# Optimization experiments

Hardware: AMD Instinct MI355X
Metric: run time of the kernel (lower is better)

The kernel has to match this reference:

```python
import jax, jax.numpy as jnp
import numpy as np

HEADS = 16

def rotate_half(t):
    t1, t2 = jnp.split(t, 2, axis=-1)
    return jnp.concatenate([-t2, t1], axis=-1)

def apply_rotary_pos_emb(pos, t):
    # pos: [N, hd] broadcasts against t: [B, H, N, hd]
    return t * jnp.cos(pos) + rotate_half(t) * jnp.sin(pos)

def setup_inputs() -> dict:
    key = jax.random.key(0)
    ks = jax.random.split(key, 6)
    B, N, D, H = 2, 2048, 1024, HEADS
    hd = D // H
    s = D ** -0.5
    x = jax.random.normal(ks[0], (B, N, D), jnp.float32)
    context = jax.random.normal(ks[1], (B, N, D), jnp.float32)
    pos_emb = jax.random.normal(ks[2], (N, hd), jnp.float32)
    Wq = jax.random.normal(ks[3], (D, D), jnp.float32) * s
    Wkv = jax.random.normal(ks[4], (D, 2 * D), jnp.float32) * s
    Wout = jax.random.normal(ks[5], (D, D), jnp.float32) * s
    b_out = jnp.zeros((D,), jnp.float32)
    return {"x": x, "context": context, "pos_emb": pos_emb,
            "Wq": Wq, "Wkv": Wkv, "Wout": Wout, "b_out": b_out}

def reference(x, context, pos_emb, Wq, Wkv, Wout, b_out):
    B, N, D = x.shape
    H = HEADS
    hd = D // H
    scale = hd ** -0.5
    # projections: [B,N,D] -> [B,H,N,hd]
    q = (x @ Wq).reshape(B, N, H, hd).transpose(0, 2, 1, 3)
    k, v = jnp.split(context @ Wkv, 2, axis=-1)
    k = k.reshape(B, N, H, hd).transpose(0, 2, 1, 3)
    v = v.reshape(B, N, H, hd).transpose(0, 2, 1, 3)
    # rotary applied to q and k just before scores
    q = apply_rotary_pos_emb(pos_emb, q)
    k = apply_rotary_pos_emb(pos_emb, k)
    dots = jnp.einsum('bhid,bhjd->bhij', q, k) * scale  # [B,H,N,N]
    attn = jax.nn.softmax(dots, axis=-1)
    out = jnp.einsum('bhij,bhjd->bhid', attn, v)
    out = out.transpose(0, 2, 1, 3).reshape(B, N, D)
    return out @ Wout + b_out
```

## Files before the change

### kernel.cpp

```cpp
#include <hip/hip_runtime.h>
#include <math.h>

#define D_MODEL 1024
#define NSEQ    2048
#define NHEADS  16
#define HD      64

typedef __attribute__((ext_vector_type(8))) short bf16x8;
typedef __attribute__((ext_vector_type(4))) float f32x4;

__device__ inline unsigned short f2bf(float x) {
    union { float f; unsigned int u; } a; a.f = x;
    unsigned int r = a.u + 0x7fffu + ((a.u >> 16) & 1u);
    return (unsigned short)(r >> 16);
}
__device__ inline float bf2f(unsigned short b) {
    union { unsigned int u; float f; } a; a.u = ((unsigned int)b) << 16;
    return a.f;
}
__device__ inline unsigned int pack2(unsigned short a, unsigned short b) {
    return (unsigned int)a | ((unsigned int)b << 16);
}
__device__ inline unsigned int cvtpk_bf16(float lo, float hi) {
    unsigned int r;
    asm volatile("v_cvt_pk_bf16_f32 %0, %1, %2" : "=v"(r) : "v"(lo), "v"(hi));
    return r;
}
__device__ inline float fexp2(float x) { return __builtin_amdgcn_exp2f(x); }
__device__ inline void async_load16(const void* g, void* l) {
    __builtin_amdgcn_global_load_lds(
        (const __attribute__((address_space(1))) unsigned int*)g,
        (__attribute__((address_space(3))) unsigned int*)l, 16, 0, 0);
}

#define QSCALE 0.180336880111112f
#define MSHIFT 12.0f

__global__ __launch_bounds__(256) void prep_kernel(
    const float* __restrict__ x, const float* __restrict__ ctx,
    const float* __restrict__ Wq, const float* __restrict__ Wkv,
    const float* __restrict__ Wout, const float* __restrict__ pos,
    unsigned short* __restrict__ AX, unsigned short* __restrict__ AC,
    unsigned short* __restrict__ WQ, unsigned short* __restrict__ WK,
    unsigned short* __restrict__ WO, float* __restrict__ ct,
    float* __restrict__ st)
{
    __shared__ float Ws[32][33];
    const int bid = blockIdx.x, tid = threadIdx.x;
    if (bid < 8192) {
        const float* src = bid < 4096 ? x : ctx;
        unsigned short* dst = bid < 4096 ? AX : AC;
        int m = bid & 4095;
        int kq = tid * 4;
        float4 v = *reinterpret_cast<const float4*>(&src[(size_t)m * 1024 + kq]);
        float vv[4] = {v.x, v.y, v.z, v.w};
        unsigned short h[4];
#pragma unroll
        for (int c = 0; c < 4; ++c) h[c] = f2bf(vv[c]);
        size_t base = (size_t)m * 2048 + kq;
        *reinterpret_cast<uint2*>(&dst[base]) =
            make_uint2(pack2(h[0], h[1]), pack2(h[2], h[3]));
    } else if (bid < 12288) {
        int t = bid - 8192;
        const float* W; unsigned short* Y; int N, tilesx;
        if (t < 1024)      { W = Wq;   Y = WQ; N = 1024; tilesx = 32; }
        else if (t < 3072) { t -= 1024; W = Wkv; Y = WK; N = 2048; tilesx = 64; }
        else               { t -= 3072; W = Wout; Y = WO; N = 1024; tilesx = 32; }
        int n0 = (t % tilesx) * 32, k0 = (t / tilesx) * 32;
        int c = tid & 31, r4 = tid >> 5;
#pragma unroll
        for (int i = 0; i < 4; ++i) {
            int r = r4 * 4 + i;
            Ws[r][c] = W[(size_t)(k0 + r) * N + n0 + c];
        }
        __syncthreads();
#pragma unroll
        for (int i = 0; i < 4; ++i) {
            int nr = r4 * 4 + i;
            Y[(size_t)(n0 + nr) * 2048 + k0 + c] = f2bf(Ws[c][nr]);
        }
    } else {
        int idx = (bid - 12288) * 256 + tid;
        float s, c;
        sincosf(pos[idx], &s, &c);
        ct[idx] = c;
        st[idx] = s;
    }
}

__global__ __launch_bounds__(512) void gemm_qkv(
    const unsigned short* __restrict__ AX, const unsigned short* __restrict__ AC,
    const unsigned short* __restrict__ WQ, const unsigned short* __restrict__ WK,
    unsigned short* __restrict__ Qb, unsigned short* __restrict__ Kb,
    unsigned short* __restrict__ Vt, const float* __restrict__ ct,
    const float* __restrict__ st)
{
    __shared__ unsigned short As[128 * 64];
    __shared__ unsigned short Bs[128 * 64];
    const int tid = threadIdx.x;
    const int l = tid & 63;
    const int wv = tid >> 6;
    const int wr  = wv >> 2;
    const int wch = (wv & 3) >> 1;
    const int whf = wv & 1;
    const int lr_ = l & 15, lg_ = l >> 4;

    const unsigned short *A, *Bt;
    int row0, col0, isQ;
    if (blockIdx.x < 256) {
        A = AX; Bt = WQ; isQ = 1;
        col0 = (blockIdx.x & 7) * 128;
        row0 = (blockIdx.x >> 3) * 128;
    } else {
        int i2 = blockIdx.x - 256;
        A = AC; Bt = WK; isQ = 0;
        int x = i2 & 7, i = i2 >> 3;
        col0 = (x * 2 + (i & 1)) * 128;
        row0 = (i >> 1) * 128;
    }

    f32x4 acc[4][2];
#pragma unroll
    for (int m = 0; m < 4; ++m)
#pragma unroll
        for (int n = 0; n < 2; ++n) acc[m][n] = (f32x4){0.f, 0.f, 0.f, 0.f};

    const int rsub = l >> 3;
    const int chst = (l & 7) ^ rsub;

    for (int k0 = 0; k0 < 1024; k0 += 64) {
        __syncthreads();
#pragma unroll
        for (int t = 0; t < 2; ++t) {
            int ci = wv * 2 + t;
            int row = ci * 8 + rsub;
            async_load16(&A[(size_t)(row0 + row) * 2048 + k0 + chst * 8],
                         &As[ci * 512]);
            async_load16(&Bt[(size_t)(col0 + row) * 2048 + k0 + chst * 8],
                         &Bs[ci * 512]);
        }
        __syncthreads();
#pragma unroll
        for (int ks = 0; ks < 2; ++ks) {
            int ch2 = (lg_ + ks * 4) ^ (lr_ & 7);
            bf16x8 af[4], bfv[2];
#pragma unroll
            for (int m = 0; m < 4; ++m)
                af[m] = *reinterpret_cast<const bf16x8*>(
                    &As[(wr * 64 + m * 16 + lr_) * 64 + ch2 * 8]);
#pragma unroll
            for (int n = 0; n < 2; ++n)
                bfv[n] = *reinterpret_cast<const bf16x8*>(
                    &Bs[(wch * 64 + whf * 16 + n * 32 + lr_) * 64 + ch2 * 8]);
#pragma unroll
            for (int m = 0; m < 4; ++m)
#pragma unroll
                for (int n = 0; n < 2; ++n)
                    acc[m][n] = __builtin_amdgcn_mfma_f32_16x16x32_bf16(
                        af[m], bfv[n], acc[m][n], 0, 0, 0);
        }
    }

    const int colw = col0 + wch * 64;
    if (isQ || colw < 1024) {
        unsigned short* dst = isQ ? Qb : Kb;
        const int hh = colw >> 6;
        const float qs = isQ ? QSCALE : 1.f;
#pragma unroll
        for (int m = 0; m < 4; ++m) {
            int grow0 = row0 + wr * 64 + m * 16 + lg_ * 4;
            int b = grow0 >> 11, nq0 = grow0 & 2047;
#pragma unroll
            for (int j = 0; j < 4; ++j) {
                int nq = nq0 + j;
                int d = whf * 16 + lr_;
                float a = acc[m][0][j], bb = acc[m][1][j];
                float c1 = ct[nq * 64 + d],      s1 = st[nq * 64 + d];
                float c2 = ct[nq * 64 + d + 32], s2 = st[nq * 64 + d + 32];
                size_t obase = (((size_t)b * 16 + hh) * 2048 + nq) * 64;
                dst[obase + d]      = f2bf((a * c1 - bb * s1) * qs);
                dst[obase + d + 32] = f2bf((bb * c2 + a * s2) * qs);
            }
        }
    } else {
        const int hh = (colw - 1024) >> 6;
#pragma unroll
        for (int m = 0; m < 4; ++m) {
            int grow0 = row0 + wr * 64 + m * 16 + lg_ * 4;
            int b = grow0 >> 11, nq0 = grow0 & 2047;
#pragma unroll
            for (int n = 0; n < 2; ++n) {
                int d = whf * 16 + n * 32 + lr_;
                unsigned int w0 = pack2(f2bf(acc[m][n][0]), f2bf(acc[m][n][1]));
                unsigned int w1 = pack2(f2bf(acc[m][n][2]), f2bf(acc[m][n][3]));
                *reinterpret_cast<uint2*>(
                    &Vt[(((size_t)b * 16 + hh) * 64 + d) * 2048 + nq0]) =
                    make_uint2(w0, w1);
            }
        }
    }
}

__global__ __launch_bounds__(512) void gemm_out(
    const unsigned short* __restrict__ A, const unsigned short* __restrict__ Bt,
    const float* __restrict__ bias, float* __restrict__ C)
{
    __shared__ unsigned short As[128 * 64];
    __shared__ unsigned short Bs[128 * 64];
    const int tid = threadIdx.x;
    const int l = tid & 63;
    const int wv = tid >> 6;
    const int wr  = wv >> 2;
    const int wch = (wv & 3) >> 1;
    const int whf = wv & 1;
    const int lr_ = l & 15, lg_ = l >> 4;
    const int col0 = (blockIdx.x & 7) * 128;
    const int row0 = (blockIdx.x >> 3) * 128;

    f32x4 acc[4][2];
#pragma unroll
    for (int m = 0; m < 4; ++m)
#pragma unroll
        for (int n = 0; n < 2; ++n) acc[m][n] = (f32x4){0.f, 0.f, 0.f, 0.f};

    const int rsub = l >> 3;
    const int chst = (l & 7) ^ rsub;

    for (int k0 = 0; k0 < 1024; k0 += 64) {
        __syncthreads();
#pragma unroll
        for (int t = 0; t < 2; ++t) {
            int ci = wv * 2 + t;
            int row = ci * 8 + rsub;
            async_load16(&A[(size_t)(row0 + row) * 2048 + k0 + chst * 8],
                         &As[ci * 512]);
            async_load16(&Bt[(size_t)(col0 + row) * 2048 + k0 + chst * 8],
                         &Bs[ci * 512]);
        }
        __syncthreads();
#pragma unroll
        for (int ks = 0; ks < 2; ++ks) {
            int ch2 = (lg_ + ks * 4) ^ (lr_ & 7);
            bf16x8 af[4], bfv[2];
#pragma unroll
            for (int m = 0; m < 4; ++m)
                af[m] = *reinterpret_cast<const bf16x8*>(
                    &As[(wr * 64 + m * 16 + lr_) * 64 + ch2 * 8]);
#pragma unroll
            for (int n = 0; n < 2; ++n)
                bfv[n] = *reinterpret_cast<const bf16x8*>(
                    &Bs[(wch * 64 + whf * 16 + n * 32 + lr_) * 64 + ch2 * 8]);
#pragma unroll
            for (int m = 0; m < 4; ++m)
#pragma unroll
                for (int n = 0; n < 2; ++n)
                    acc[m][n] = __builtin_amdgcn_mfma_f32_16x16x32_bf16(
                        af[m], bfv[n], acc[m][n], 0, 0, 0);
        }
    }

#pragma unroll
    for (int m = 0; m < 4; ++m) {
        int grow0 = row0 + wr * 64 + m * 16 + lg_ * 4;
#pragma unroll
        for (int n = 0; n < 2; ++n) {
            int gcol = col0 + wch * 64 + whf * 16 + n * 32 + lr_;
            float bv = bias[gcol];
#pragma unroll
            for (int j = 0; j < 4; ++j)
                C[(size_t)(grow0 + j) * 1024 + gcol] = acc[m][n][j] + bv;
        }
    }
}

__global__ __launch_bounds__(512) void flash_mfma(
    const unsigned short* __restrict__ Qb, const unsigned short* __restrict__ Kb,
    const unsigned short* __restrict__ Vt, unsigned short* __restrict__ Oa)
{
    __shared__ unsigned short Ks[2][4096];
    __shared__ unsigned short Vs[2][4096];
    __shared__ unsigned short Ps[8][1024];

    const int tid = threadIdx.x;
    const int l = tid & 63;
    const int w = tid >> 6;
    const int lg = l >> 4;
    const int lr = l & 15;
    const int bh = blockIdx.y;
    const int q0 = blockIdx.x * 128;

    bf16x8 qf[2];
    {
        const unsigned short* qp =
            Qb + ((size_t)bh * NSEQ + q0 + w * 16 + lr) * HD + lg * 8;
        qf[0] = *reinterpret_cast<const bf16x8*>(qp);
        qf[1] = *reinterpret_cast<const bf16x8*>(qp + 32);
    }

    f32x4 oacc[4];
#pragma unroll
    for (int j = 0; j < 4; ++j) oacc[j] = (f32x4){0.f, 0.f, 0.f, 0.f};
    float l_i = 0.f;

    unsigned short* pw = Ps[w];

    const int r_  = tid >> 3;
    const int ch_ = (tid & 7) ^ (r_ & 7);
    const unsigned short* kPtr = Kb + ((size_t)bh * NSEQ + r_) * HD + ch_ * 8;
    const unsigned short* vPtr = Vt + ((size_t)bh * HD + r_) * NSEQ + ch_ * 8;

#define STAGE(b) do {                              \
    async_load16(kPtr, &Ks[b][w * 512]);           \
    async_load16(vPtr, &Vs[b][w * 512]);           \
    kPtr += 64 * HD; vPtr += 64;                   \
} while (0)

#define COMPUTE(b) do {                                                        \
    f32x4 sacc[4];                                                             \
    _Pragma("unroll")                                                          \
    for (int n = 0; n < 4; ++n)                                                \
        sacc[n] = (f32x4){-MSHIFT, -MSHIFT, -MSHIFT, -MSHIFT};                 \
    __builtin_amdgcn_s_setprio(1);                                             \
    _Pragma("unroll")                                                          \
    for (int ks = 0; ks < 2; ++ks)                                             \
        _Pragma("unroll")                                                      \
        for (int n = 0; n < 4; ++n) {                                          \
            int kr = n * 16 + lr;                                              \
            int ch = (lg + ks * 4) ^ (kr & 7);                                 \
            bf16x8 kf = *reinterpret_cast<const bf16x8*>(                      \
                &Ks[b][kr * 64 + ch * 8]);                                     \
            sacc[n] = __builtin_amdgcn_mfma_f32_16x16x32_bf16(                 \
                kf, qf[ks], sacc[n], 0, 0, 0);                                 \
        }                                                                      \
    __builtin_amdgcn_s_setprio(0);                                             \
    float p[4][4];                                                             \
    float sum = 0.f;                                                           \
    _Pragma("unroll")                                                          \
    for (int n = 0; n < 4; ++n)                                                \
        _Pragma("unroll")                                                      \
        for (int j = 0; j < 4; ++j) {                                          \
            p[n][j] = fexp2(sacc[n][j]);                                       \
            sum += p[n][j];                                                    \
        }                                                                      \
    sum += __shfl_xor(sum, 16);                                                \
    sum += __shfl_xor(sum, 32);                                                \
    l_i += sum;                                                                \
    _Pragma("unroll")                                                          \
    for (int n = 0; n < 4; ++n) {                                              \
        unsigned int u0 = cvtpk_bf16(p[n][0], p[n][1]);                        \
        unsigned int u1 = cvtpk_bf16(p[n][2], p[n][3]);                        \
        int swc = (2 * n + (lg >> 1)) ^ (lr & 7);                              \
        *reinterpret_cast<uint2*>(&pw[lr * 64 + swc * 8 + 4 * (lg & 1)]) =     \
            make_uint2(u0, u1);                                                \
    }                                                                          \
    asm volatile("s_waitcnt lgkmcnt(0)" ::: "memory");                         \
    __builtin_amdgcn_s_setprio(1);                                             \
    _Pragma("unroll")                                                          \
    for (int ks = 0; ks < 2; ++ks) {                                           \
        int pch = (lg + 4 * ks) ^ (lr & 7);                                    \
        bf16x8 pf = *reinterpret_cast<const bf16x8*>(                          \
            &pw[lr * 64 + pch * 8]);                                           \
        _Pragma("unroll")                                                      \
        for (int dt = 0; dt < 4; ++dt) {                                       \
            int d = dt * 16 + lr;                                              \
            int ch = (lg + ks * 4) ^ (d & 7);                                  \
            bf16x8 vf = *reinterpret_cast<const bf16x8*>(                      \
                &Vs[b][d * 64 + ch * 8]);                                      \
            oacc[dt] = __builtin_amdgcn_mfma_f32_16x16x32_bf16(                \
                pf, vf, oacc[dt], 0, 0, 0);                                    \
        }                                                                      \
    }                                                                          \
    __builtin_amdgcn_s_setprio(0);                                             \
} while (0)

    STAGE(0);
    asm volatile("s_waitcnt vmcnt(0)" ::: "memory");
    __syncthreads();

    for (int jt = 0; jt < NSEQ / 64; jt += 2) {
        STAGE(1);
        COMPUTE(0);
        asm volatile("s_waitcnt vmcnt(0)" ::: "memory");
        __syncthreads();
        if (jt + 2 < NSEQ / 64) STAGE(0);
        COMPUTE(1);
        asm volatile("s_waitcnt vmcnt(0)" ::: "memory");
        __syncthreads();
    }
#undef STAGE
#undef COMPUTE

    const int b = bh >> 4, h = bh & 15;
#pragma unroll
    for (int j = 0; j < 4; ++j) {
        float lj = __shfl(l_i, (l & 48) | (lg * 4 + j));
        float inv = 1.f / lj;
        int nq = q0 + w * 16 + lg * 4 + j;
        size_t rbase = ((size_t)b * NSEQ + nq) * 2048 + h * 64;
#pragma unroll
        for (int dt = 0; dt < 4; ++dt)
            Oa[rbase + dt * 16 + lr] = f2bf(oacc[dt][j] * inv);
    }
}

__global__ __launch_bounds__(256) void sgemm_kernel(
    const float* __restrict__ A, const float* __restrict__ B,
    const float* __restrict__ bias, float* __restrict__ C,
    int M, int N, int K)
{
    __shared__ float As[16][132];
    __shared__ float Bs[16][132];
    const int tid = threadIdx.x;
    const int tr = tid >> 4;
    const int tc = tid & 15;
    const int arow0 = blockIdx.y * 128;
    const int bcol0 = blockIdx.x * 128;
    float acc[8][8];
#pragma unroll
    for (int i = 0; i < 8; ++i)
#pragma unroll
        for (int j = 0; j < 8; ++j) acc[i][j] = 0.f;
    for (int k0 = 0; k0 < K; k0 += 16) {
#pragma unroll
        for (int t = 0; t < 2; ++t) {
            int f = tid + t * 256;
            int row = f >> 2, kg = f & 3;
            float4 av = *reinterpret_cast<const float4*>(
                &A[(size_t)(arow0 + row) * K + k0 + kg * 4]);
            As[kg * 4 + 0][row] = av.x;
            As[kg * 4 + 1][row] = av.y;
            As[kg * 4 + 2][row] = av.z;
            As[kg * 4 + 3][row] = av.w;
        }
#pragma unroll
        for (int t = 0; t < 2; ++t) {
            int f = tid + t * 256;
            int kr = f >> 5, cg = f & 31;
            *reinterpret_cast<float4*>(&Bs[kr][cg * 4]) =
                *reinterpret_cast<const float4*>(
                    &B[(size_t)(k0 + kr) * N + bcol0 + cg * 4]);
        }
        __syncthreads();
#pragma unroll
        for (int kk = 0; kk < 16; ++kk) {
            float a[8], b[8];
            *reinterpret_cast<float4*>(&a[0]) = *reinterpret_cast<const float4*>(&As[kk][tr * 4]);
            *reinterpret_cast<float4*>(&a[4]) = *reinterpret_cast<const float4*>(&As[kk][64 + tr * 4]);
            *reinterpret_cast<float4*>(&b[0]) = *reinterpret_cast<const float4*>(&Bs[kk][tc * 4]);
            *reinterpret_cast<float4*>(&b[4]) = *reinterpret_cast<const float4*>(&Bs[kk][64 + tc * 4]);
#pragma unroll
            for (int i = 0; i < 8; ++i)
#pragma unroll
                for (int j = 0; j < 8; ++j) acc[i][j] = fmaf(a[i], b[j], acc[i][j]);
        }
        __syncthreads();
    }
#pragma unroll
    for (int i = 0; i < 8; ++i) {
        int row = arow0 + ((i < 4) ? (tr * 4 + i) : (64 + tr * 4 + i - 4));
#pragma unroll
        for (int jh = 0; jh < 2; ++jh) {
            int col = bcol0 + ((jh == 0) ? (tc * 4) : (64 + tc * 4));
            float4 v;
            v.x = acc[i][jh * 4 + 0];
            v.y = acc[i][jh * 4 + 1];
            v.z = acc[i][jh * 4 + 2];
            v.w = acc[i][jh * 4 + 3];
            if (bias) {
                v.x += bias[col + 0]; v.y += bias[col + 1];
                v.z += bias[col + 2]; v.w += bias[col + 3];
            }
            *reinterpret_cast<float4*>(&C[(size_t)row * N + col]) = v;
        }
    }
}

__global__ void rope_kernel(float* __restrict__ t, const float* __restrict__ pos,
                            int rowstride)
{
    int idx = blockIdx.x * 256 + threadIdx.x;
    int d = idx & 31;
    int h = (idx >> 5) & (NHEADS - 1);
    int m = idx >> 9;
    int n = m & (NSEQ - 1);
    float p1 = pos[n * HD + d];
    float p2 = pos[n * HD + 32 + d];
    size_t base = (size_t)m * rowstride + h * HD;
    float a = t[base + d];
    float b = t[base + 32 + d];
    float s1, c1, s2, c2;
    sincosf(p1, &s1, &c1);
    sincosf(p2, &s2, &c2);
    t[base + d]      = a * c1 - b * s1;
    t[base + 32 + d] = b * c2 + a * s2;
}

__global__ __launch_bounds__(256) void flash_kernel(
    const float* __restrict__ q, const float* __restrict__ kv,
    float* __restrict__ o)
{
    __shared__ float Qs[64][68];
    __shared__ float Kt[64][68];
    __shared__ float Vs2[64][68];

    const int rb = blockIdx.x;
    const int bh = blockIdx.y;
    const int b = bh >> 4;
    const int h = bh & (NHEADS - 1);
    const int tid = threadIdx.x;
    const int tr = tid >> 4;
    const int tc = tid & 15;

#pragma unroll
    for (int t = 0; t < 4; ++t) {
        int f = tid + t * 256;
        int row = f >> 4, cg = f & 15;
        *reinterpret_cast<float4*>(&Qs[row][cg * 4]) =
            *reinterpret_cast<const float4*>(
                &q[((size_t)(b * NSEQ + rb * 64 + row)) * D_MODEL + h * HD + cg * 4]);
    }

    float m_i[4], l_i[4], oacc[4][4];
#pragma unroll
    for (int i = 0; i < 4; ++i) {
        m_i[i] = -INFINITY; l_i[i] = 0.f;
#pragma unroll
        for (int j = 0; j < 4; ++j) oacc[i][j] = 0.f;
    }

    float (*Ps2)[68] = Kt;

    for (int jt = 0; jt < NSEQ / 64; ++jt) {
        __syncthreads();
#pragma unroll
        for (int t = 0; t < 4; ++t) {
            int f = tid + t * 256;
            int row = f >> 4, cg = f & 15;
            size_t base = ((size_t)(b * NSEQ + jt * 64 + row)) * (2 * D_MODEL) + h * HD + cg * 4;
            float4 kq = *reinterpret_cast<const float4*>(&kv[base]);
            float4 vv = *reinterpret_cast<const float4*>(&kv[base + D_MODEL]);
            Kt[cg * 4 + 0][row] = kq.x;
            Kt[cg * 4 + 1][row] = kq.y;
            Kt[cg * 4 + 2][row] = kq.z;
            Kt[cg * 4 + 3][row] = kq.w;
            *reinterpret_cast<float4*>(&Vs2[row][cg * 4]) = vv;
        }
        __syncthreads();

        float s[4][4];
#pragma unroll
        for (int i = 0; i < 4; ++i)
#pragma unroll
            for (int j = 0; j < 4; ++j) s[i][j] = 0.f;
        for (int dg = 0; dg < 16; ++dg) {
            float Qv[4][4];
#pragma unroll
            for (int i = 0; i < 4; ++i)
                *reinterpret_cast<float4*>(Qv[i]) =
                    *reinterpret_cast<const float4*>(&Qs[tr * 4 + i][dg * 4]);
#pragma unroll
            for (int dd = 0; dd < 4; ++dd) {
                float ka[4];
                *reinterpret_cast<float4*>(ka) =
                    *reinterpret_cast<const float4*>(&Kt[dg * 4 + dd][tc * 4]);
#pragma unroll
                for (int i = 0; i < 4; ++i)
#pragma unroll
                    for (int j = 0; j < 4; ++j)
                        s[i][j] = fmaf(Qv[i][dd], ka[j], s[i][j]);
            }
        }

#pragma unroll
        for (int i = 0; i < 4; ++i) {
            float tmax = -INFINITY;
#pragma unroll
            for (int j = 0; j < 4; ++j) {
                s[i][j] *= 0.125f;
                tmax = fmaxf(tmax, s[i][j]);
            }
#pragma unroll
            for (int msk = 1; msk < 16; msk <<= 1)
                tmax = fmaxf(tmax, __shfl_xor(tmax, msk, 16));
            float mnew = fmaxf(m_i[i], tmax);
            float corr = expf(m_i[i] - mnew);
            float tsum = 0.f;
#pragma unroll
            for (int j = 0; j < 4; ++j) {
                s[i][j] = expf(s[i][j] - mnew);
                tsum += s[i][j];
            }
#pragma unroll
            for (int msk = 1; msk < 16; msk <<= 1)
                tsum += __shfl_xor(tsum, msk, 16);
            l_i[i] = l_i[i] * corr + tsum;
            m_i[i] = mnew;
#pragma unroll
            for (int j = 0; j < 4; ++j) oacc[i][j] *= corr;
        }

        __syncthreads();
#pragma unroll
        for (int i = 0; i < 4; ++i) {
            float4 v;
            v.x = s[i][0]; v.y = s[i][1]; v.z = s[i][2]; v.w = s[i][3];
            *reinterpret_cast<float4*>(&Ps2[tr * 4 + i][tc * 4]) = v;
        }
        __syncthreads();

        for (int cg = 0; cg < 16; ++cg) {
            float P_[4][4], V_[4][4];
#pragma unroll
            for (int i = 0; i < 4; ++i)
                *reinterpret_cast<float4*>(P_[i]) =
                    *reinterpret_cast<const float4*>(&Ps2[tr * 4 + i][cg * 4]);
#pragma unroll
            for (int c = 0; c < 4; ++c)
                *reinterpret_cast<float4*>(V_[c]) =
                    *reinterpret_cast<const float4*>(&Vs2[cg * 4 + c][tc * 4]);
#pragma unroll
            for (int i = 0; i < 4; ++i)
#pragma unroll
                for (int c = 0; c < 4; ++c)
#pragma unroll
                    for (int j = 0; j < 4; ++j)
                        oacc[i][j] = fmaf(P_[i][c], V_[c][j], oacc[i][j]);
        }
    }

#pragma unroll
    for (int i = 0; i < 4; ++i) {
        float inv = 1.f / l_i[i];
        float4 v;
        v.x = oacc[i][0] * inv; v.y = oacc[i][1] * inv;
        v.z = oacc[i][2] * inv; v.w = oacc[i][3] * inv;
        *reinterpret_cast<float4*>(
            &o[((size_t)(b * NSEQ + rb * 64 + tr * 4 + i)) * D_MODEL + h * HD + tc * 4]) = v;
    }
}

extern "C" void kernel_launch(void* const* d_in, const int* in_sizes, int n_in,
                              void* d_out, int out_size, void* d_ws, size_t ws_size,
                              hipStream_t stream) {
    const float* x       = (const float*)d_in[0];
    const float* context = (const float*)d_in[1];
    const float* pos     = (const float*)d_in[2];
    const float* Wq      = (const float*)d_in[3];
    const float* Wkv     = (const float*)d_in[4];
    const float* Wout    = (const float*)d_in[5];
    const float* b_out   = (const float*)d_in[6];
    float* out = (float*)d_out;

    const int M = 2 * NSEQ;
    dim3 blk(256);

    const size_t NEED = 76546048ULL;
    if (ws_size >= NEED) {
        unsigned short* AX = (unsigned short*)d_ws;
        unsigned short* AC = AX + 8388608;
        unsigned short* WQ = AC + 8388608;
        unsigned short* WK = WQ + 2097152;
        unsigned short* WO = WK + 4194304;
        unsigned short* Qb = WO + 2097152;
        unsigned short* Kb = Qb + 4194304;
        unsigned short* Vt = Kb + 4194304;
        float* ct = (float*)(Vt + 4194304);
        float* st = ct + 131072;

        prep_kernel<<<12800, blk, 0, stream>>>(
            x, context, Wq, Wkv, Wout, pos, AX, AC, WQ, WK, WO, ct, st);
        gemm_qkv<<<768, dim3(512), 0, stream>>>(AX, AC, WQ, WK, Qb, Kb, Vt, ct, st);
        flash_mfma<<<dim3(NSEQ / 128, 32), dim3(512), 0, stream>>>(Qb, Kb, Vt, AX);
        gemm_out<<<256, dim3(512), 0, stream>>>(AX, WO, b_out, out);
    } else {
        float* ws = (float*)d_ws;
        float* q  = ws;
        float* kv = q + (size_t)M * D_MODEL;
        float* o  = kv + (size_t)M * 2 * D_MODEL;
        sgemm_kernel<<<dim3(D_MODEL / 128, M / 128), blk, 0, stream>>>(
            x, Wq, nullptr, q, M, D_MODEL, D_MODEL);
        sgemm_kernel<<<dim3(2 * D_MODEL / 128, M / 128), blk, 0, stream>>>(
            context, Wkv, nullptr, kv, M, 2 * D_MODEL, D_MODEL);
        rope_kernel<<<(M * NHEADS * 32) / 256, blk, 0, stream>>>(q, pos, D_MODEL);
        rope_kernel<<<(M * NHEADS * 32) / 256, blk, 0, stream>>>(kv, pos, 2 * D_MODEL);
        flash_kernel<<<dim3(NSEQ / 64, 2 * NHEADS), blk, 0, stream>>>(q, kv, o);
        sgemm_kernel<<<dim3(D_MODEL / 128, M / 128), blk, 0, stream>>>(
            o, Wout, b_out, out, M, D_MODEL, D_MODEL);
    }
}
```

Measured before the change: 122.8 us.

## Triple-buffer flash K/V loads with single barrier; shrink out-proj GEMM tiles

The attention kernel now uses three shared K/V buffers and a partial vmcnt wait with one barrier per tile, so global loads for the next tile stay in flight while the current tile computes. This removes the full drain and double barrier per iteration. The output projection GEMM switches from 128x128 tiles with 512 threads to 64x64 tiles with 256 threads and four times as many blocks, to fill more CUs. The trade-off is more shared memory per flash block and less data reuse in the GEMM.

After: 118.0 us. 1.04x faster.

```diff
diff --git a/kernel.cpp b/kernel.cpp
--- a/kernel.cpp
+++ b/kernel.cpp
@@ -201,25 +201,24 @@
     }
 }
 
-__global__ __launch_bounds__(512) void gemm_out(
+__global__ __launch_bounds__(256) void gemm_out(
     const unsigned short* __restrict__ A, const unsigned short* __restrict__ Bt,
     const float* __restrict__ bias, float* __restrict__ C)
 {
-    __shared__ unsigned short As[128 * 64];
-    __shared__ unsigned short Bs[128 * 64];
+    __shared__ unsigned short As[64 * 64];
+    __shared__ unsigned short Bs[64 * 64];
     const int tid = threadIdx.x;
     const int l = tid & 63;
     const int wv = tid >> 6;
-    const int wr  = wv >> 2;
-    const int wch = (wv & 3) >> 1;
-    const int whf = wv & 1;
+    const int wr = wv >> 1;
+    const int wp = wv & 1;
     const int lr_ = l & 15, lg_ = l >> 4;
-    const int col0 = (blockIdx.x & 7) * 128;
-    const int row0 = (blockIdx.x >> 3) * 128;
-
-    f32x4 acc[4][2];
-#pragma unroll
-    for (int m = 0; m < 4; ++m)
+    const int row0 = (blockIdx.x >> 4) * 64;
+    const int col0 = (blockIdx.x & 15) * 64;
+
+    f32x4 acc[2][2];
+#pragma unroll
+    for (int m = 0; m < 2; ++m)
 #pragma unroll
         for (int n = 0; n < 2; ++n) acc[m][n] = (f32x4){0.f, 0.f, 0.f, 0.f};
 
@@ -230,7 +229,7 @@
         __syncthreads();
 #pragma unroll
         for (int t = 0; t < 2; ++t) {
-            int ci = wv * 2 + t;
+            int ci = wv + 4 * t;
             int row = ci * 8 + rsub;
             async_load16(&A[(size_t)(row0 + row) * 2048 + k0 + chst * 8],
                          &As[ci * 512]);
@@ -241,17 +240,17 @@
 #pragma unroll
         for (int ks = 0; ks < 2; ++ks) {
             int ch2 = (lg_ + ks * 4) ^ (lr_ & 7);
-            bf16x8 af[4], bfv[2];
-#pragma unroll
-            for (int m = 0; m < 4; ++m)
+            bf16x8 af[2], bfv[2];
+#pragma unroll
+            for (int m = 0; m < 2; ++m)
                 af[m] = *reinterpret_cast<const bf16x8*>(
-                    &As[(wr * 64 + m * 16 + lr_) * 64 + ch2 * 8]);
+                    &As[(wr * 32 + m * 16 + lr_) * 64 + ch2 * 8]);
 #pragma unroll
             for (int n = 0; n < 2; ++n)
                 bfv[n] = *reinterpret_cast<const bf16x8*>(
-                    &Bs[(wch * 64 + whf * 16 + n * 32 + lr_) * 64 + ch2 * 8]);
-#pragma unroll
-            for (int m = 0; m < 4; ++m)
+                    &Bs[(wp * 16 + n * 32 + lr_) * 64 + ch2 * 8]);
+#pragma unroll
+            for (int m = 0; m < 2; ++m)
 #pragma unroll
                 for (int n = 0; n < 2; ++n)
                     acc[m][n] = __builtin_amdgcn_mfma_f32_16x16x32_bf16(
@@ -260,11 +259,11 @@
     }
 
 #pragma unroll
-    for (int m = 0; m < 4; ++m) {
-        int grow0 = row0 + wr * 64 + m * 16 + lg_ * 4;
+    for (int m = 0; m < 2; ++m) {
+        int grow0 = row0 + wr * 32 + m * 16 + lg_ * 4;
 #pragma unroll
         for (int n = 0; n < 2; ++n) {
-            int gcol = col0 + wch * 64 + whf * 16 + n * 32 + lr_;
+            int gcol = col0 + wp * 16 + n * 32 + lr_;
             float bv = bias[gcol];
 #pragma unroll
             for (int j = 0; j < 4; ++j)
@@ -277,8 +276,8 @@
     const unsigned short* __restrict__ Qb, const unsigned short* __restrict__ Kb,
     const unsigned short* __restrict__ Vt, unsigned short* __restrict__ Oa)
 {
-    __shared__ unsigned short Ks[2][4096];
-    __shared__ unsigned short Vs[2][4096];
+    __shared__ unsigned short Ks[3][4096];
+    __shared__ unsigned short Vs[3][4096];
     __shared__ unsigned short Ps[8][1024];
 
     const int tid = threadIdx.x;
@@ -313,6 +312,12 @@
     async_load16(kPtr, &Ks[b][w * 512]);           \
     async_load16(vPtr, &Vs[b][w * 512]);           \
     kPtr += 64 * HD; vPtr += 64;                   \
+} while (0)
+
+#define WAITBAR2 do {                                              \
+    asm volatile("s_waitcnt vmcnt(2)" ::: "memory");               \
+    __builtin_amdgcn_s_barrier();                                  \
+    __builtin_amdgcn_sched_barrier(0);                             \
 } while (0)
 
 #define COMPUTE(b) do {                                                        \
@@ -354,6 +359,7 @@
             make_uint2(u0, u1);                                                \
     }                                                                          \
     asm volatile("s_waitcnt lgkmcnt(0)" ::: "memory");                         \
+    __builtin_amdgcn_sched_barrier(0);                                         \
     __builtin_amdgcn_s_setprio(1);                                             \
     _Pragma("unroll")                                                          \
     for (int ks = 0; ks < 2; ++ks) {                                           \
@@ -374,20 +380,18 @@
 } while (0)
 
     STAGE(0);
+    for (int base = 0; base < 30; base += 3) {
+        STAGE(1); WAITBAR2; COMPUTE(0);
+        STAGE(2); WAITBAR2; COMPUTE(1);
+        STAGE(0); WAITBAR2; COMPUTE(2);
+    }
+    STAGE(1); WAITBAR2; COMPUTE(0);
     asm volatile("s_waitcnt vmcnt(0)" ::: "memory");
-    __syncthreads();
-
-    for (int jt = 0; jt < NSEQ / 64; jt += 2) {
-        STAGE(1);
-        COMPUTE(0);
-        asm volatile("s_waitcnt vmcnt(0)" ::: "memory");
-        __syncthreads();
-        if (jt + 2 < NSEQ / 64) STAGE(0);
-        COMPUTE(1);
-        asm volatile("s_waitcnt vmcnt(0)" ::: "memory");
-        __syncthreads();
-    }
+    __builtin_amdgcn_s_barrier();
+    __builtin_amdgcn_sched_barrier(0);
+    COMPUTE(1);
 #undef STAGE
+#undef WAITBAR2
 #undef COMPUTE
 
     const int b = bh >> 4, h = bh & 15;
@@ -671,7 +675,7 @@
             x, context, Wq, Wkv, Wout, pos, AX, AC, WQ, WK, WO, ct, st);
         gemm_qkv<<<768, dim3(512), 0, stream>>>(AX, AC, WQ, WK, Qb, Kb, Vt, ct, st);
         flash_mfma<<<dim3(NSEQ / 128, 32), dim3(512), 0, stream>>>(Qb, Kb, Vt, AX);
-        gemm_out<<<256, dim3(512), 0, stream>>>(AX, WO, b_out, out);
+        gemm_out<<<1024, blk, 0, stream>>>(AX, WO, b_out, out);
     } else {
         float* ws = (float*)d_ws;
         float* q  = ws;
```
